# Kernel optimization log

Measured on AMD Instinct MI355X. Metric: run time of the kernel, lower is better.

The kernel has to match this reference:

```python
import jax, jax.numpy as jnp
import numpy as np

N_HEADS = 16

def setup_inputs() -> dict:
    key = jax.random.key(0)
    ks = jax.random.split(key, 7)
    B, S, D = 2, 2048, 1024
    sc = 1.0 / np.sqrt(D)
    return {
        "x": jax.random.normal(ks[0], (B, S, D), dtype=jnp.float32),
        "Wq": jax.random.normal(ks[1], (D, D), dtype=jnp.float32) * sc,
        "bq": jax.random.normal(ks[2], (D,), dtype=jnp.float32) * 0.02,
        "Wk": jax.random.normal(ks[3], (D, D), dtype=jnp.float32) * sc,
        "bk": jax.random.normal(ks[4], (D,), dtype=jnp.float32) * 0.02,
        "Wv": jax.random.normal(ks[5], (D, D), dtype=jnp.float32) * sc,
        "bv": jax.random.normal(ks[6], (D,), dtype=jnp.float32) * 0.02,
    }

def reference(x, Wq, bq, Wk, bk, Wv, bv):
    B, S, D = x.shape
    H = N_HEADS
    W = D // H  # head width
    # QKV projections (torch Linear: x @ W^T + b); here weights stored as [D_in, D_out]
    q = x @ Wq + bq
    k = x @ Wk + bk
    v = x @ Wv + bv
    # split last dim into heads -> [B, H, S, W]
    q = q.reshape(B, S, H, W).transpose(0, 2, 1, 3)
    k = k.reshape(B, S, H, W).transpose(0, 2, 1, 3)
    v = v.reshape(B, S, H, W).transpose(0, 2, 1, 3)
    # scaled dot-product attention; full [B,H,S,S] scores as in original
    scores = jnp.einsum("bhqw,bhkw->bhqk", q, k) / jnp.sqrt(jnp.asarray(W, x.dtype))
    probs = jax.nn.softmax(scores, axis=-1)  # dropout is identity in eval mode
    h = jnp.einsum("bhqk,bhkw->bhqw", probs, v)
    # merge heads -> [B, S, D]
    return h.transpose(0, 2, 1, 3).reshape(B, S, D)
```

## Files before the change

kernel.cpp:

```cpp
#include <hip/hip_runtime.h>

typedef _Float16 H16;
typedef _Float16 half8 __attribute__((ext_vector_type(8)));
typedef _Float16 half4 __attribute__((ext_vector_type(4)));
typedef float f32x4 __attribute__((ext_vector_type(4)));

constexpr int Bb = 2, S = 2048, D = 1024, NH = 16, HW = 64;
constexpr int M = Bb * S;

constexpr size_t XH_OFF = 0;
constexpr size_t WT_OFF = XH_OFF + (size_t)M * D * 2;
constexpr size_t Q_OFF  = WT_OFF + 3ull * D * D * 2;
constexpr size_t K_OFF  = Q_OFF + (size_t)M * D * 2;
constexpr size_t VT_OFF = K_OFF + (size_t)M * D * 2;

#define GLOAD_LDS16(g, l)                                        \
  __builtin_amdgcn_global_load_lds(                              \
      (const __attribute__((address_space(1))) void*)(g),        \
      (__attribute__((address_space(3))) void*)(l), 16, 0, 0)

__global__ __launch_bounds__(256) void cvt_x(const float* __restrict__ x,
                                             H16* __restrict__ xh) {
  size_t i = ((size_t)blockIdx.x * 256 + threadIdx.x) * 8;
  float4 a = *(const float4*)(x + i);
  float4 b = *(const float4*)(x + i + 4);
  half8 h = {(H16)a.x, (H16)a.y, (H16)a.z, (H16)a.w,
             (H16)b.x, (H16)b.y, (H16)b.z, (H16)b.w};
  *(half8*)(xh + i) = h;
}

__global__ __launch_bounds__(256) void wt_cvt(const float* __restrict__ w0,
                                              const float* __restrict__ w1,
                                              const float* __restrict__ w2,
                                              H16* __restrict__ wt) {
  __shared__ H16 tile[64][65];
  const float* w = blockIdx.z == 0 ? w0 : blockIdx.z == 1 ? w1 : w2;
  H16* out = wt + (size_t)blockIdx.z * D * D;
  int t = threadIdx.x;
  int c = t & 63, r4 = t >> 6;
  int bx = blockIdx.x * 64, by = blockIdx.y * 64;
#pragma unroll 4
  for (int it = 0; it < 16; ++it) {
    int row = it * 4 + r4;
    tile[c][row] = (H16)w[(size_t)(by + row) * D + bx + c];
  }
  __syncthreads();
#pragma unroll 4
  for (int it = 0; it < 16; ++it) {
    int row = it * 4 + r4;
    out[(size_t)(bx + row) * D + by + c] = tile[row][c];
  }
}

__global__ __launch_bounds__(256) void qkv_gemm(
    const H16* __restrict__ xh, const H16* __restrict__ wt,
    const float* __restrict__ bq, const float* __restrict__ bk,
    const float* __restrict__ bv, H16* __restrict__ qo, H16* __restrict__ ko,
    H16* __restrict__ vto) {
  __shared__ __align__(16) H16 As[128 * 32];
  __shared__ __align__(16) H16 Bs[128 * 32];
  const int z = blockIdx.z;
  const H16* w = wt + (size_t)z * D * D;
  const float* bias = z == 0 ? bq : z == 1 ? bk : bv;
  const int bm = blockIdx.y * 128, bn = blockIdx.x * 128;
  const int t = threadIdx.x;
  const int wave = t >> 6, lane = t & 63;
  const int g = lane >> 4, c = lane & 15;
  const int wm = (wave >> 1) * 64, wn = (wave & 1) * 64;

  f32x4 acc[4][4] = {};

  for (int kk = 0; kk < D; kk += 32) {
#pragma unroll
    for (int rnd = 0; rnd < 2; ++rnd) {
      int cid = rnd * 256 + t;
      int row = cid >> 2, k0 = (cid & 3) * 8;
      GLOAD_LDS16(&xh[(size_t)(bm + row) * D + kk + k0], &As[cid * 8]);
      GLOAD_LDS16(&w[(size_t)(bn + row) * D + kk + k0], &Bs[cid * 8]);
    }
    __syncthreads();
    half8 af[4], bf[4];
#pragma unroll
    for (int i = 0; i < 4; ++i) {
      af[i] = *(const half8*)&As[(wm + i * 16 + c) * 32 + g * 8];
      bf[i] = *(const half8*)&Bs[(wn + i * 16 + c) * 32 + g * 8];
    }
#pragma unroll
    for (int i = 0; i < 4; ++i)
#pragma unroll
      for (int j = 0; j < 4; ++j)
        acc[i][j] =
            __builtin_amdgcn_mfma_f32_16x16x32_f16(af[i], bf[j], acc[i][j], 0, 0, 0);
    __syncthreads();
  }

#pragma unroll
  for (int i = 0; i < 4; ++i) {
#pragma unroll
    for (int j = 0; j < 4; ++j) {
      int coln = bn + wn + j * 16 + c;
      float bse = bias[coln];
      int h = coln >> 6, wcol = coln & 63;
      if (z == 2) {
        int row0 = bm + wm + i * 16 + g * 4;
        int bbx = row0 >> 11, s0 = row0 & (S - 1);
        half4 v4 = {(H16)(acc[i][j][0] + bse), (H16)(acc[i][j][1] + bse),
                    (H16)(acc[i][j][2] + bse), (H16)(acc[i][j][3] + bse)};
        *(half4*)&vto[((size_t)(bbx * NH + h) * HW + wcol) * S + s0] = v4;
      } else {
#pragma unroll
        for (int r = 0; r < 4; ++r) {
          int row = bm + wm + i * 16 + g * 4 + r;
          float val = acc[i][j][r] + bse;
          int bbx = row >> 11, s = row & (S - 1);
          size_t bh = (size_t)(bbx * NH + h);
          if (z == 0)
            qo[(bh * S + s) * HW + wcol] = (H16)val;
          else
            ko[(bh * S + s) * HW + wcol] = (H16)val;
        }
      }
    }
  }
}

__global__ __launch_bounds__(256, 3) void attn(const H16* __restrict__ q,
                                               const H16* __restrict__ k,
                                               const H16* __restrict__ vt,
                                               float* __restrict__ out) {
  constexpr int PSTR = 72;
  __shared__ __align__(16) H16 Ks[2][64 * 64];
  __shared__ __align__(16) H16 Vs[2][64 * 64];
  __shared__ __align__(16) H16 pl[4][32 * PSTR];

  const int id = blockIdx.x;
  const int xcd = id & 7, slot = id >> 3;
  const int bh = xcd * 4 + (slot >> 4);
  const int qt = slot & 15;

  const int t = threadIdx.x, wave = t >> 6, lane = t & 63;
  const int g = lane >> 4, c = lane & 15;
  const int q0 = qt * 128 + wave * 32;
  const H16* qp = q + ((size_t)bh * S + q0) * HW;
  const H16* kp = k + (size_t)bh * S * HW;
  const H16* vp = vt + (size_t)bh * HW * S;

  const int r0 = t >> 3, k8 = t & 7;
  const int r1 = r0 + 32;
  const int wsw0 = r0 * 64 + ((k8 ^ (r0 & 7)) * 8);
  const int wsw1 = r1 * 64 + ((k8 ^ (r1 & 7)) * 8);

  half8 qb[2][2];
#pragma unroll
  for (int qg = 0; qg < 2; ++qg) {
    qb[qg][0] = *(const half8*)&qp[(qg * 16 + c) * HW + g * 8];
    qb[qg][1] = *(const half8*)&qp[(qg * 16 + c) * HW + 32 + g * 8];
  }

  f32x4 o[4][2] = {};
  float l[2] = {0.f, 0.f};
  const float sc = 0.125f * 1.44269504088896f;
  H16* myp = pl[wave];

  const int sw0 = (g ^ (c & 7)) * 8;
  const int sw1 = ((4 + g) ^ (c & 7)) * 8;

  {
    half8 ka = *(const half8*)&kp[(size_t)r0 * HW + k8 * 8];
    half8 kb = *(const half8*)&kp[(size_t)r1 * HW + k8 * 8];
    half8 va = *(const half8*)&vp[(size_t)r0 * S + k8 * 8];
    half8 vb = *(const half8*)&vp[(size_t)r1 * S + k8 * 8];
    *(half8*)&Ks[0][wsw0] = ka;
    *(half8*)&Ks[0][wsw1] = kb;
    *(half8*)&Vs[0][wsw0] = va;
    *(half8*)&Vs[0][wsw1] = vb;
  }

  int buf = 0;
  for (int it = 0; it < S / 64; ++it) {
    __syncthreads();

    half8 nka, nkb, nva, nvb;
    if (it + 1 < S / 64) {
      const int nck = (it + 1) * 64;
      nka = *(const half8*)&kp[(size_t)(nck + r0) * HW + k8 * 8];
      nkb = *(const half8*)&kp[(size_t)(nck + r1) * HW + k8 * 8];
      nva = *(const half8*)&vp[(size_t)r0 * S + nck + k8 * 8];
      nvb = *(const half8*)&vp[(size_t)r1 * S + nck + k8 * 8];
    }

    const H16* ks = Ks[buf];
    const H16* vs = Vs[buf];

    f32x4 st[4][2];
#pragma unroll
    for (int kt = 0; kt < 4; ++kt) {
      const H16* kr = &ks[(kt * 16 + c) * 64];
      half8 ka0 = *(const half8*)&kr[sw0];
      half8 ka1 = *(const half8*)&kr[sw1];
#pragma unroll
      for (int qg = 0; qg < 2; ++qg) {
        f32x4 z = {};
        st[kt][qg] =
            __builtin_amdgcn_mfma_f32_16x16x32_f16(ka0, qb[qg][0], z, 0, 0, 0);
        st[kt][qg] = __builtin_amdgcn_mfma_f32_16x16x32_f16(ka1, qb[qg][1],
                                                            st[kt][qg], 0, 0, 0);
      }
    }

    half8 pb[2][2];
#pragma unroll
    for (int qg = 0; qg < 2; ++qg) {
#pragma unroll
      for (int kt = 0; kt < 4; ++kt) {
        float p0 = __builtin_amdgcn_exp2f(st[kt][qg][0] * sc);
        float p1 = __builtin_amdgcn_exp2f(st[kt][qg][1] * sc);
        float p2 = __builtin_amdgcn_exp2f(st[kt][qg][2] * sc);
        float p3 = __builtin_amdgcn_exp2f(st[kt][qg][3] * sc);
        l[qg] += (p0 + p1) + (p2 + p3);
        half4 pk = {(H16)p0, (H16)p1, (H16)p2, (H16)p3};
        *(half4*)&myp[(qg * 16 + c) * PSTR + kt * 16 + g * 4] = pk;
      }
      pb[qg][0] = *(const half8*)&myp[(qg * 16 + c) * PSTR + g * 8];
      pb[qg][1] = *(const half8*)&myp[(qg * 16 + c) * PSTR + 32 + g * 8];
    }

#pragma unroll
    for (int wt = 0; wt < 4; ++wt) {
      const H16* vr = &vs[(wt * 16 + c) * 64];
      half8 va0 = *(const half8*)&vr[sw0];
      half8 va1 = *(const half8*)&vr[sw1];
#pragma unroll
      for (int qg = 0; qg < 2; ++qg) {
        o[wt][qg] = __builtin_amdgcn_mfma_f32_16x16x32_f16(va0, pb[qg][0],
                                                           o[wt][qg], 0, 0, 0);
        o[wt][qg] = __builtin_amdgcn_mfma_f32_16x16x32_f16(va1, pb[qg][1],
                                                           o[wt][qg], 0, 0, 0);
      }
    }

    if (it + 1 < S / 64) {
      H16* kd = Ks[buf ^ 1];
      H16* vd = Vs[buf ^ 1];
      *(half8*)&kd[wsw0] = nka;
      *(half8*)&kd[wsw1] = nkb;
      *(half8*)&vd[wsw0] = nva;
      *(half8*)&vd[wsw1] = nvb;
    }
    buf ^= 1;
  }

#pragma unroll
  for (int qg = 0; qg < 2; ++qg) {
    l[qg] += __shfl_xor(l[qg], 16, 64);
    l[qg] += __shfl_xor(l[qg], 32, 64);
  }

  const int bbx = bh >> 4, h = bh & 15;
#pragma unroll
  for (int qg = 0; qg < 2; ++qg) {
    const float inv = 1.0f / l[qg];
    float* orow = out + ((size_t)bbx * S + q0 + qg * 16 + c) * D + h * HW;
#pragma unroll
    for (int wt = 0; wt < 4; ++wt) {
      float4 v4 = {o[wt][qg][0] * inv, o[wt][qg][1] * inv, o[wt][qg][2] * inv,
                   o[wt][qg][3] * inv};
      *(float4*)&orow[wt * 16 + g * 4] = v4;
    }
  }
}

extern "C" void kernel_launch(void* const* d_in, const int* in_sizes, int n_in,
                              void* d_out, int out_size, void* d_ws,
                              size_t ws_size, hipStream_t stream) {
  const float* x = (const float*)d_in[0];
  const float* Wq = (const float*)d_in[1];
  const float* bq = (const float*)d_in[2];
  const float* Wk = (const float*)d_in[3];
  const float* bk = (const float*)d_in[4];
  const float* Wv = (const float*)d_in[5];
  const float* bv = (const float*)d_in[6];
  float* out = (float*)d_out;
  char* ws = (char*)d_ws;
  H16* xh = (H16*)(ws + XH_OFF);
  H16* wt = (H16*)(ws + WT_OFF);
  H16* qw = (H16*)(ws + Q_OFF);
  H16* kw = (H16*)(ws + K_OFF);
  H16* vtw = (H16*)(ws + VT_OFF);

  cvt_x<<<dim3((M * D) / (256 * 8)), 256, 0, stream>>>(x, xh);
  wt_cvt<<<dim3(16, 16, 3), 256, 0, stream>>>(Wq, Wk, Wv, wt);
  qkv_gemm<<<dim3(8, 32, 3), 256, 0, stream>>>(xh, wt, bq, bk, bv, qw, kw, vtw);
  attn<<<dim3(512), 256, 0, stream>>>(qw, kw, vtw, out);
}
```

Measured before the change: 169.5 us.

## Software-pipeline QK^T one tile ahead with triple-buffered V in attention

The attention loop now computes the score MFMAs for the next K tile while the exp/softmax and PV MFMAs of the current tile run, so the matrix and vector work can overlap. Global prefetch is pushed two tiles ahead, and V gets a third LDS buffer so the tile still being read is not overwritten. The occupancy hint drops from 3 to 2 blocks per SM to make room for the extra score registers. This trades lower occupancy and more LDS for more instruction-level parallelism inside each wave.

```diff
diff --git a/kernel.cpp b/kernel.cpp
--- a/kernel.cpp
+++ b/kernel.cpp
@@ -124,13 +124,14 @@
   }
 }
 
-__global__ __launch_bounds__(256, 3) void attn(const H16* __restrict__ q,
+__global__ __launch_bounds__(256, 2) void attn(const H16* __restrict__ q,
                                                const H16* __restrict__ k,
                                                const H16* __restrict__ vt,
                                                float* __restrict__ out) {
   constexpr int PSTR = 72;
+  constexpr int NIT = S / 64;
   __shared__ __align__(16) H16 Ks[2][64 * 64];
-  __shared__ __align__(16) H16 Vs[2][64 * 64];
+  __shared__ __align__(16) H16 Vs[3][64 * 64];
   __shared__ __align__(16) H16 pl[4][32 * PSTR];
 
   const int id = blockIdx.x;
@@ -165,46 +166,64 @@
   const int sw0 = (g ^ (c & 7)) * 8;
   const int sw1 = ((4 + g) ^ (c & 7)) * 8;
 
-  {
-    half8 ka = *(const half8*)&kp[(size_t)r0 * HW + k8 * 8];
-    half8 kb = *(const half8*)&kp[(size_t)r1 * HW + k8 * 8];
-    half8 va = *(const half8*)&vp[(size_t)r0 * S + k8 * 8];
-    half8 vb = *(const half8*)&vp[(size_t)r1 * S + k8 * 8];
-    *(half8*)&Ks[0][wsw0] = ka;
-    *(half8*)&Ks[0][wsw1] = kb;
-    *(half8*)&Vs[0][wsw0] = va;
-    *(half8*)&Vs[0][wsw1] = vb;
-  }
-
-  int buf = 0;
-  for (int it = 0; it < S / 64; ++it) {
+#pragma unroll
+  for (int pc = 0; pc < 2; ++pc) {
+    const int ck = pc * 64;
+    half8 ka = *(const half8*)&kp[(size_t)(ck + r0) * HW + k8 * 8];
+    half8 kb = *(const half8*)&kp[(size_t)(ck + r1) * HW + k8 * 8];
+    half8 va = *(const half8*)&vp[(size_t)r0 * S + ck + k8 * 8];
+    half8 vb = *(const half8*)&vp[(size_t)r1 * S + ck + k8 * 8];
+    *(half8*)&Ks[pc][wsw0] = ka;
+    *(half8*)&Ks[pc][wsw1] = kb;
+    *(half8*)&Vs[pc][wsw0] = va;
+    *(half8*)&Vs[pc][wsw1] = vb;
+  }
+  __syncthreads();
+
+  f32x4 stp[4][2];
+#pragma unroll
+  for (int kt = 0; kt < 4; ++kt) {
+    const H16* kr = &Ks[0][(kt * 16 + c) * 64];
+    half8 ka0 = *(const half8*)&kr[sw0];
+    half8 ka1 = *(const half8*)&kr[sw1];
+#pragma unroll
+    for (int qg = 0; qg < 2; ++qg) {
+      f32x4 z = {};
+      stp[kt][qg] =
+          __builtin_amdgcn_mfma_f32_16x16x32_f16(ka0, qb[qg][0], z, 0, 0, 0);
+      stp[kt][qg] = __builtin_amdgcn_mfma_f32_16x16x32_f16(ka1, qb[qg][1],
+                                                           stp[kt][qg], 0, 0, 0);
+    }
+  }
+
+  for (int it = 0; it < NIT; ++it) {
     __syncthreads();
 
     half8 nka, nkb, nva, nvb;
-    if (it + 1 < S / 64) {
-      const int nck = (it + 1) * 64;
+    if (it + 2 < NIT) {
+      const int nck = (it + 2) * 64;
       nka = *(const half8*)&kp[(size_t)(nck + r0) * HW + k8 * 8];
       nkb = *(const half8*)&kp[(size_t)(nck + r1) * HW + k8 * 8];
       nva = *(const half8*)&vp[(size_t)r0 * S + nck + k8 * 8];
       nvb = *(const half8*)&vp[(size_t)r1 * S + nck + k8 * 8];
     }
 
-    const H16* ks = Ks[buf];
-    const H16* vs = Vs[buf];
-
-    f32x4 st[4][2];
-#pragma unroll
-    for (int kt = 0; kt < 4; ++kt) {
-      const H16* kr = &ks[(kt * 16 + c) * 64];
-      half8 ka0 = *(const half8*)&kr[sw0];
-      half8 ka1 = *(const half8*)&kr[sw1];
-#pragma unroll
-      for (int qg = 0; qg < 2; ++qg) {
-        f32x4 z = {};
-        st[kt][qg] =
-            __builtin_amdgcn_mfma_f32_16x16x32_f16(ka0, qb[qg][0], z, 0, 0, 0);
-        st[kt][qg] = __builtin_amdgcn_mfma_f32_16x16x32_f16(ka1, qb[qg][1],
-                                                            st[kt][qg], 0, 0, 0);
+    f32x4 stn[4][2];
+    if (it + 1 < NIT) {
+      const H16* ks = Ks[(it + 1) & 1];
+#pragma unroll
+      for (int kt = 0; kt < 4; ++kt) {
+        const H16* kr = &ks[(kt * 16 + c) * 64];
+        half8 ka0 = *(const half8*)&kr[sw0];
+        half8 ka1 = *(const half8*)&kr[sw1];
+#pragma unroll
+        for (int qg = 0; qg < 2; ++qg) {
+          f32x4 z = {};
+          stn[kt][qg] =
+              __builtin_amdgcn_mfma_f32_16x16x32_f16(ka0, qb[qg][0], z, 0, 0, 0);
+          stn[kt][qg] = __builtin_amdgcn_mfma_f32_16x16x32_f16(
+              ka1, qb[qg][1], stn[kt][qg], 0, 0, 0);
+        }
       }
     }
 
@@ -213,10 +232,10 @@
     for (int qg = 0; qg < 2; ++qg) {
 #pragma unroll
       for (int kt = 0; kt < 4; ++kt) {
-        float p0 = __builtin_amdgcn_exp2f(st[kt][qg][0] * sc);
-        float p1 = __builtin_amdgcn_exp2f(st[kt][qg][1] * sc);
-        float p2 = __builtin_amdgcn_exp2f(st[kt][qg][2] * sc);
-        float p3 = __builtin_amdgcn_exp2f(st[kt][qg][3] * sc);
+        float p0 = __builtin_amdgcn_exp2f(stp[kt][qg][0] * sc);
+        float p1 = __builtin_amdgcn_exp2f(stp[kt][qg][1] * sc);
+        float p2 = __builtin_amdgcn_exp2f(stp[kt][qg][2] * sc);
+        float p3 = __builtin_amdgcn_exp2f(stp[kt][qg][3] * sc);
         l[qg] += (p0 + p1) + (p2 + p3);
         half4 pk = {(H16)p0, (H16)p1, (H16)p2, (H16)p3};
         *(half4*)&myp[(qg * 16 + c) * PSTR + kt * 16 + g * 4] = pk;
@@ -225,6 +244,7 @@
       pb[qg][1] = *(const half8*)&myp[(qg * 16 + c) * PSTR + 32 + g * 8];
     }
 
+    const H16* vs = Vs[it % 3];
 #pragma unroll
     for (int wt = 0; wt < 4; ++wt) {
       const H16* vr = &vs[(wt * 16 + c) * 64];
@@ -239,15 +259,21 @@
       }
     }
 
-    if (it + 1 < S / 64) {
-      H16* kd = Ks[buf ^ 1];
-      H16* vd = Vs[buf ^ 1];
+    if (it + 2 < NIT) {
+      H16* kd = Ks[it & 1];
+      H16* vd = Vs[(it + 2) % 3];
       *(half8*)&kd[wsw0] = nka;
       *(half8*)&kd[wsw1] = nkb;
       *(half8*)&vd[wsw0] = nva;
       *(half8*)&vd[wsw1] = nvb;
     }
-    buf ^= 1;
+
+    if (it + 1 < NIT) {
+#pragma unroll
+      for (int kt = 0; kt < 4; ++kt)
+#pragma unroll
+        for (int qg = 0; qg < 2; ++qg) stp[kt][qg] = stn[kt][qg];
+    }
   }
 
 #pragma unroll
```

After: 166.8 us. About the same (-1.6%).

## Load V fragments directly from global into registers, drop V LDS staging

Applied to the files above, without the earlier changes.

V^T fragments are now loaded straight from global memory into registers, double-buffered across a manually unrolled pair of iterations, so V no longer goes through shared memory. The softmax scale is folded into Q once at load time, removing a multiply per score. The P scratch buffer now uses an XOR swizzle instead of padding. Launch bounds drop to 2 blocks per CU to make room for the extra V registers, which may cut occupancy. Each wave now fetches V itself rather than sharing one LDS copy across the block, and pre-scaling Q in fp16 adds rounding error.

```diff
diff --git a/kernel.cpp b/kernel.cpp
--- a/kernel.cpp
+++ b/kernel.cpp
@@ -124,14 +124,13 @@
   }
 }
 
-__global__ __launch_bounds__(256, 3) void attn(const H16* __restrict__ q,
+__global__ __launch_bounds__(256, 2) void attn(const H16* __restrict__ q,
                                                const H16* __restrict__ k,
                                                const H16* __restrict__ vt,
                                                float* __restrict__ out) {
-  constexpr int PSTR = 72;
+  constexpr int NIT = S / 64;
   __shared__ __align__(16) H16 Ks[2][64 * 64];
-  __shared__ __align__(16) H16 Vs[2][64 * 64];
-  __shared__ __align__(16) H16 pl[4][32 * PSTR];
+  __shared__ __align__(16) H16 pl[4][32 * 64];
 
   const int id = blockIdx.x;
   const int xcd = id & 7, slot = id >> 3;
@@ -150,105 +149,109 @@
   const int wsw0 = r0 * 64 + ((k8 ^ (r0 & 7)) * 8);
   const int wsw1 = r1 * 64 + ((k8 ^ (r1 & 7)) * 8);
 
+  const H16 scq = (H16)(0.125f * 1.44269504088896f);
   half8 qb[2][2];
 #pragma unroll
   for (int qg = 0; qg < 2; ++qg) {
     qb[qg][0] = *(const half8*)&qp[(qg * 16 + c) * HW + g * 8];
     qb[qg][1] = *(const half8*)&qp[(qg * 16 + c) * HW + 32 + g * 8];
+#pragma unroll
+    for (int e = 0; e < 8; ++e) {
+      qb[qg][0][e] *= scq;
+      qb[qg][1][e] *= scq;
+    }
   }
 
   f32x4 o[4][2] = {};
   float l[2] = {0.f, 0.f};
-  const float sc = 0.125f * 1.44269504088896f;
   H16* myp = pl[wave];
 
   const int sw0 = (g ^ (c & 7)) * 8;
   const int sw1 = ((4 + g) ^ (c & 7)) * 8;
+  int pwc[4];
+#pragma unroll
+  for (int kt = 0; kt < 4; ++kt)
+    pwc[kt] = (((kt * 2 + (g >> 1)) ^ (c & 7)) * 8) + (g & 1) * 4;
+
+  const H16* vrow[4];
+#pragma unroll
+  for (int wt = 0; wt < 4; ++wt) vrow[wt] = vp + (size_t)(wt * 16 + c) * S;
 
   {
     half8 ka = *(const half8*)&kp[(size_t)r0 * HW + k8 * 8];
     half8 kb = *(const half8*)&kp[(size_t)r1 * HW + k8 * 8];
-    half8 va = *(const half8*)&vp[(size_t)r0 * S + k8 * 8];
-    half8 vb = *(const half8*)&vp[(size_t)r1 * S + k8 * 8];
     *(half8*)&Ks[0][wsw0] = ka;
     *(half8*)&Ks[0][wsw1] = kb;
-    *(half8*)&Vs[0][wsw0] = va;
-    *(half8*)&Vs[0][wsw1] = vb;
-  }
-
-  int buf = 0;
-  for (int it = 0; it < S / 64; ++it) {
-    __syncthreads();
-
-    half8 nka, nkb, nva, nvb;
-    if (it + 1 < S / 64) {
-      const int nck = (it + 1) * 64;
-      nka = *(const half8*)&kp[(size_t)(nck + r0) * HW + k8 * 8];
-      nkb = *(const half8*)&kp[(size_t)(nck + r1) * HW + k8 * 8];
-      nva = *(const half8*)&vp[(size_t)r0 * S + nck + k8 * 8];
-      nvb = *(const half8*)&vp[(size_t)r1 * S + nck + k8 * 8];
-    }
-
-    const H16* ks = Ks[buf];
-    const H16* vs = Vs[buf];
-
-    f32x4 st[4][2];
-#pragma unroll
-    for (int kt = 0; kt < 4; ++kt) {
-      const H16* kr = &ks[(kt * 16 + c) * 64];
-      half8 ka0 = *(const half8*)&kr[sw0];
-      half8 ka1 = *(const half8*)&kr[sw1];
-#pragma unroll
-      for (int qg = 0; qg < 2; ++qg) {
-        f32x4 z = {};
-        st[kt][qg] =
-            __builtin_amdgcn_mfma_f32_16x16x32_f16(ka0, qb[qg][0], z, 0, 0, 0);
-        st[kt][qg] = __builtin_amdgcn_mfma_f32_16x16x32_f16(ka1, qb[qg][1],
-                                                            st[kt][qg], 0, 0, 0);
-      }
-    }
-
-    half8 pb[2][2];
-#pragma unroll
-    for (int qg = 0; qg < 2; ++qg) {
-#pragma unroll
-      for (int kt = 0; kt < 4; ++kt) {
-        float p0 = __builtin_amdgcn_exp2f(st[kt][qg][0] * sc);
-        float p1 = __builtin_amdgcn_exp2f(st[kt][qg][1] * sc);
-        float p2 = __builtin_amdgcn_exp2f(st[kt][qg][2] * sc);
-        float p3 = __builtin_amdgcn_exp2f(st[kt][qg][3] * sc);
-        l[qg] += (p0 + p1) + (p2 + p3);
-        half4 pk = {(H16)p0, (H16)p1, (H16)p2, (H16)p3};
-        *(half4*)&myp[(qg * 16 + c) * PSTR + kt * 16 + g * 4] = pk;
-      }
-      pb[qg][0] = *(const half8*)&myp[(qg * 16 + c) * PSTR + g * 8];
-      pb[qg][1] = *(const half8*)&myp[(qg * 16 + c) * PSTR + 32 + g * 8];
-    }
-
-#pragma unroll
-    for (int wt = 0; wt < 4; ++wt) {
-      const H16* vr = &vs[(wt * 16 + c) * 64];
-      half8 va0 = *(const half8*)&vr[sw0];
-      half8 va1 = *(const half8*)&vr[sw1];
-#pragma unroll
-      for (int qg = 0; qg < 2; ++qg) {
-        o[wt][qg] = __builtin_amdgcn_mfma_f32_16x16x32_f16(va0, pb[qg][0],
-                                                           o[wt][qg], 0, 0, 0);
-        o[wt][qg] = __builtin_amdgcn_mfma_f32_16x16x32_f16(va1, pb[qg][1],
-                                                           o[wt][qg], 0, 0, 0);
-      }
-    }
-
-    if (it + 1 < S / 64) {
-      H16* kd = Ks[buf ^ 1];
-      H16* vd = Vs[buf ^ 1];
-      *(half8*)&kd[wsw0] = nka;
-      *(half8*)&kd[wsw1] = nkb;
-      *(half8*)&vd[wsw0] = nva;
-      *(half8*)&vd[wsw1] = nvb;
-    }
-    buf ^= 1;
-  }
+  }
+  half8 vA[4][2], vB[4][2];
+#pragma unroll
+  for (int wt = 0; wt < 4; ++wt) {
+    vA[wt][0] = *(const half8*)&vrow[wt][g * 8];
+    vA[wt][1] = *(const half8*)&vrow[wt][32 + g * 8];
+  }
+
+#define ATTN_ITER(IT, VCUR, VNXT, PAR)                                        \
+  {                                                                           \
+    __syncthreads();                                                          \
+    const bool more = (IT) + 1 < NIT;                                         \
+    const int nck = ((IT) + 1) * 64;                                          \
+    half8 nka, nkb;                                                           \
+    if (more) {                                                               \
+      nka = *(const half8*)&kp[(size_t)(nck + r0) * HW + k8 * 8];             \
+      nkb = *(const half8*)&kp[(size_t)(nck + r1) * HW + k8 * 8];             \
+      _Pragma("unroll") for (int wt = 0; wt < 4; ++wt) {                      \
+        VNXT[wt][0] = *(const half8*)&vrow[wt][nck + g * 8];                  \
+        VNXT[wt][1] = *(const half8*)&vrow[wt][nck + 32 + g * 8];             \
+      }                                                                       \
+    }                                                                         \
+    const H16* ks = Ks[PAR];                                                  \
+    f32x4 st[4][2];                                                           \
+    _Pragma("unroll") for (int kt = 0; kt < 4; ++kt) {                        \
+      const H16* kr = &ks[(kt * 16 + c) * 64];                                \
+      half8 ka0 = *(const half8*)&kr[sw0];                                    \
+      half8 ka1 = *(const half8*)&kr[sw1];                                    \
+      _Pragma("unroll") for (int qg = 0; qg < 2; ++qg) {                      \
+        f32x4 zz = {};                                                        \
+        st[kt][qg] = __builtin_amdgcn_mfma_f32_16x16x32_f16(                  \
+            ka0, qb[qg][0], zz, 0, 0, 0);                                     \
+        st[kt][qg] = __builtin_amdgcn_mfma_f32_16x16x32_f16(                  \
+            ka1, qb[qg][1], st[kt][qg], 0, 0, 0);                             \
+      }                                                                       \
+    }                                                                         \
+    half8 pb[2][2];                                                           \
+    _Pragma("unroll") for (int qg = 0; qg < 2; ++qg) {                        \
+      _Pragma("unroll") for (int kt = 0; kt < 4; ++kt) {                      \
+        float p0 = __builtin_amdgcn_exp2f(st[kt][qg][0]);                     \
+        float p1 = __builtin_amdgcn_exp2f(st[kt][qg][1]);                     \
+        float p2 = __builtin_amdgcn_exp2f(st[kt][qg][2]);                     \
+        float p3 = __builtin_amdgcn_exp2f(st[kt][qg][3]);                     \
+        l[qg] += (p0 + p1) + (p2 + p3);                                       \
+        half4 pk = {(H16)p0, (H16)p1, (H16)p2, (H16)p3};                      \
+        *(half4*)&myp[(qg * 16 + c) * 64 + pwc[kt]] = pk;                     \
+      }                                                                       \
+      pb[qg][0] = *(const half8*)&myp[(qg * 16 + c) * 64 + sw0];              \
+      pb[qg][1] = *(const half8*)&myp[(qg * 16 + c) * 64 + sw1];              \
+    }                                                                         \
+    _Pragma("unroll") for (int wt = 0; wt < 4; ++wt) {                        \
+      _Pragma("unroll") for (int qg = 0; qg < 2; ++qg) {                      \
+        o[wt][qg] = __builtin_amdgcn_mfma_f32_16x16x32_f16(                   \
+            VCUR[wt][0], pb[qg][0], o[wt][qg], 0, 0, 0);                      \
+        o[wt][qg] = __builtin_amdgcn_mfma_f32_16x16x32_f16(                   \
+            VCUR[wt][1], pb[qg][1], o[wt][qg], 0, 0, 0);                      \
+      }                                                                       \
+    }                                                                         \
+    if (more) {                                                               \
+      H16* kd = Ks[(PAR) ^ 1];                                                \
+      *(half8*)&kd[wsw0] = nka;                                               \
+      *(half8*)&kd[wsw1] = nkb;                                               \
+    }                                                                         \
+  }
+
+  for (int itp = 0; itp < NIT; itp += 2) {
+    ATTN_ITER(itp, vA, vB, 0)
+    ATTN_ITER(itp + 1, vB, vA, 1)
+  }
+#undef ATTN_ITER
 
 #pragma unroll
   for (int qg = 0; qg < 2; ++qg) {
```

New measurement: 190.0 us. +12.1%, slower.

## Merge conversion kernels, fold softmax scale into Q, swizzle P buffer

Applied to the files above, without the earlier changes.

The x fp16 conversion and the weight transpose-convert are merged into one launch that uses a z slice for x, removing one kernel launch. In attention the softmax scale is multiplied into Q once in fp16 instead of on every score. The padded P staging buffer is replaced by an XOR-swizzled unpadded layout, and the occupancy hint drops from 3 to 2 blocks per SM. Scaling Q in fp16 adds rounding error, and the lower occupancy hint may reduce latency hiding but allows more registers.

```diff
diff --git a/kernel.cpp b/kernel.cpp
--- a/kernel.cpp
+++ b/kernel.cpp
@@ -19,36 +19,42 @@
       (const __attribute__((address_space(1))) void*)(g),        \
       (__attribute__((address_space(3))) void*)(l), 16, 0, 0)
 
-__global__ __launch_bounds__(256) void cvt_x(const float* __restrict__ x,
-                                             H16* __restrict__ xh) {
-  size_t i = ((size_t)blockIdx.x * 256 + threadIdx.x) * 8;
-  float4 a = *(const float4*)(x + i);
-  float4 b = *(const float4*)(x + i + 4);
-  half8 h = {(H16)a.x, (H16)a.y, (H16)a.z, (H16)a.w,
-             (H16)b.x, (H16)b.y, (H16)b.z, (H16)b.w};
-  *(half8*)(xh + i) = h;
-}
-
-__global__ __launch_bounds__(256) void wt_cvt(const float* __restrict__ w0,
-                                              const float* __restrict__ w1,
-                                              const float* __restrict__ w2,
-                                              H16* __restrict__ wt) {
+__global__ __launch_bounds__(256) void prep(const float* __restrict__ x,
+                                            H16* __restrict__ xh,
+                                            const float* __restrict__ w0,
+                                            const float* __restrict__ w1,
+                                            const float* __restrict__ w2,
+                                            H16* __restrict__ wt) {
   __shared__ H16 tile[64][65];
-  const float* w = blockIdx.z == 0 ? w0 : blockIdx.z == 1 ? w1 : w2;
-  H16* out = wt + (size_t)blockIdx.z * D * D;
-  int t = threadIdx.x;
-  int c = t & 63, r4 = t >> 6;
-  int bx = blockIdx.x * 64, by = blockIdx.y * 64;
+  const int z = blockIdx.z;
+  const int t = threadIdx.x;
+  if (z == 0) {
+    const int bid = blockIdx.y * 16 + blockIdx.x;
+#pragma unroll
+    for (int r = 0; r < 8; ++r) {
+      size_t i = ((size_t)(bid * 8 + r) * 256 + t) * 8;
+      float4 a = *(const float4*)(x + i);
+      float4 b = *(const float4*)(x + i + 4);
+      half8 h = {(H16)a.x, (H16)a.y, (H16)a.z, (H16)a.w,
+                 (H16)b.x, (H16)b.y, (H16)b.z, (H16)b.w};
+      *(half8*)(xh + i) = h;
+    }
+  } else {
+    const float* w = z == 1 ? w0 : z == 2 ? w1 : w2;
+    H16* out = wt + (size_t)(z - 1) * D * D;
+    int c = t & 63, r4 = t >> 6;
+    int bx = blockIdx.x * 64, by = blockIdx.y * 64;
 #pragma unroll 4
-  for (int it = 0; it < 16; ++it) {
-    int row = it * 4 + r4;
-    tile[c][row] = (H16)w[(size_t)(by + row) * D + bx + c];
-  }
-  __syncthreads();
+    for (int it = 0; it < 16; ++it) {
+      int row = it * 4 + r4;
+      tile[c][row] = (H16)w[(size_t)(by + row) * D + bx + c];
+    }
+    __syncthreads();
 #pragma unroll 4
-  for (int it = 0; it < 16; ++it) {
-    int row = it * 4 + r4;
-    out[(size_t)(bx + row) * D + by + c] = tile[row][c];
+    for (int it = 0; it < 16; ++it) {
+      int row = it * 4 + r4;
+      out[(size_t)(bx + row) * D + by + c] = tile[row][c];
+    }
   }
 }
 
@@ -124,14 +130,14 @@
   }
 }
 
-__global__ __launch_bounds__(256, 3) void attn(const H16* __restrict__ q,
+__global__ __launch_bounds__(256, 2) void attn(const H16* __restrict__ q,
                                                const H16* __restrict__ k,
                                                const H16* __restrict__ vt,
                                                float* __restrict__ out) {
-  constexpr int PSTR = 72;
+  constexpr int NIT = S / 64;
   __shared__ __align__(16) H16 Ks[2][64 * 64];
   __shared__ __align__(16) H16 Vs[2][64 * 64];
-  __shared__ __align__(16) H16 pl[4][32 * PSTR];
+  __shared__ __align__(16) H16 pl[4][32 * 64];
 
   const int id = blockIdx.x;
   const int xcd = id & 7, slot = id >> 3;
@@ -150,20 +156,29 @@
   const int wsw0 = r0 * 64 + ((k8 ^ (r0 & 7)) * 8);
   const int wsw1 = r1 * 64 + ((k8 ^ (r1 & 7)) * 8);
 
+  const H16 scq = (H16)(0.125f * 1.44269504088896f);
   half8 qb[2][2];
 #pragma unroll
   for (int qg = 0; qg < 2; ++qg) {
     qb[qg][0] = *(const half8*)&qp[(qg * 16 + c) * HW + g * 8];
     qb[qg][1] = *(const half8*)&qp[(qg * 16 + c) * HW + 32 + g * 8];
+#pragma unroll
+    for (int e = 0; e < 8; ++e) {
+      qb[qg][0][e] *= scq;
+      qb[qg][1][e] *= scq;
+    }
   }
 
   f32x4 o[4][2] = {};
   float l[2] = {0.f, 0.f};
-  const float sc = 0.125f * 1.44269504088896f;
   H16* myp = pl[wave];
 
   const int sw0 = (g ^ (c & 7)) * 8;
   const int sw1 = ((4 + g) ^ (c & 7)) * 8;
+  int pwc[4];
+#pragma unroll
+  for (int kt = 0; kt < 4; ++kt)
+    pwc[kt] = (((kt * 2 + (g >> 1)) ^ (c & 7)) * 8) + (g & 1) * 4;
 
   {
     half8 ka = *(const half8*)&kp[(size_t)r0 * HW + k8 * 8];
@@ -177,11 +192,11 @@
   }
 
   int buf = 0;
-  for (int it = 0; it < S / 64; ++it) {
+  for (int it = 0; it < NIT; ++it) {
     __syncthreads();
 
     half8 nka, nkb, nva, nvb;
-    if (it + 1 < S / 64) {
+    if (it + 1 < NIT) {
       const int nck = (it + 1) * 64;
       nka = *(const half8*)&kp[(size_t)(nck + r0) * HW + k8 * 8];
       nkb = *(const half8*)&kp[(size_t)(nck + r1) * HW + k8 * 8];
@@ -213,16 +228,16 @@
     for (int qg = 0; qg < 2; ++qg) {
 #pragma unroll
       for (int kt = 0; kt < 4; ++kt) {
-        float p0 = __builtin_amdgcn_exp2f(st[kt][qg][0] * sc);
-        float p1 = __builtin_amdgcn_exp2f(st[kt][qg][1] * sc);
-        float p2 = __builtin_amdgcn_exp2f(st[kt][qg][2] * sc);
-        float p3 = __builtin_amdgcn_exp2f(st[kt][qg][3] * sc);
+        float p0 = __builtin_amdgcn_exp2f(st[kt][qg][0]);
+        float p1 = __builtin_amdgcn_exp2f(st[kt][qg][1]);
+        float p2 = __builtin_amdgcn_exp2f(st[kt][qg][2]);
+        float p3 = __builtin_amdgcn_exp2f(st[kt][qg][3]);
         l[qg] += (p0 + p1) + (p2 + p3);
         half4 pk = {(H16)p0, (H16)p1, (H16)p2, (H16)p3};
-        *(half4*)&myp[(qg * 16 + c) * PSTR + kt * 16 + g * 4] = pk;
+        *(half4*)&myp[(qg * 16 + c) * 64 + pwc[kt]] = pk;
       }
-      pb[qg][0] = *(const half8*)&myp[(qg * 16 + c) * PSTR + g * 8];
-      pb[qg][1] = *(const half8*)&myp[(qg * 16 + c) * PSTR + 32 + g * 8];
+      pb[qg][0] = *(const half8*)&myp[(qg * 16 + c) * 64 + sw0];
+      pb[qg][1] = *(const half8*)&myp[(qg * 16 + c) * 64 + sw1];
     }
 
 #pragma unroll
@@ -239,7 +254,7 @@
       }
     }
 
-    if (it + 1 < S / 64) {
+    if (it + 1 < NIT) {
       H16* kd = Ks[buf ^ 1];
       H16* vd = Vs[buf ^ 1];
       *(half8*)&kd[wsw0] = nka;
@@ -288,8 +303,7 @@
   H16* kw = (H16*)(ws + K_OFF);
   H16* vtw = (H16*)(ws + VT_OFF);
 
-  cvt_x<<<dim3((M * D) / (256 * 8)), 256, 0, stream>>>(x, xh);
-  wt_cvt<<<dim3(16, 16, 3), 256, 0, stream>>>(Wq, Wk, Wv, wt);
+  prep<<<dim3(16, 16, 4), 256, 0, stream>>>(x, xh, Wq, Wk, Wv, wt);
   qkv_gemm<<<dim3(8, 32, 3), 256, 0, stream>>>(xh, wt, bq, bk, bv, qw, kw, vtw);
   attn<<<dim3(512), 256, 0, stream>>>(qw, kw, vtw, out);
 }
```

Result: faster. 166.0 us (-2.1%).
